# Kernel tuning notes

Hardware: AMD Instinct MI355X
Metric: run time of the kernel (lower is better)

## Reference

```python
import jax, jax.numpy as jnp
import numpy as np
import math

EMBED_DIM = 128
SCALE = math.sqrt(EMBED_DIM)


def setup_inputs() -> dict:
    key = jax.random.key(0)
    # x: [B, N, D, L] = [4, 16, 128, 2048]
    x = jax.random.normal(key, (4, 16, 128, 2048), dtype=jnp.float32)
    return {"x": x}


def reference(x):
    # x: [B, N, D, L] -> [B, N, L, D]
    xt = jnp.swapaxes(x, -1, -2)
    # scores: [B, N, L, L] = softmax(x x^T / sqrt(D))
    scores = jnp.einsum("bnld,bnmd->bnlm", xt, xt) / jnp.asarray(SCALE, xt.dtype)
    attn = jax.nn.softmax(scores, axis=-1)
    # weighted values then mean over query positions L -> [B, N, D]
    out = jnp.einsum("bnlm,bnmd->bnld", attn, xt).mean(axis=2)
    return out
```

## Files before the change

### kernel.cpp

```cpp
#include <hip/hip_runtime.h>
#include <hip/hip_fp16.h>

#define H_  64
#define D_  128
#define L_  2048
#define PRE 0.35709578f

typedef _Float16 half8 __attribute__((ext_vector_type(8)));
typedef float    f32x4 __attribute__((ext_vector_type(4)));

__device__ __forceinline__ float fast_exp2(float x) {
#if __has_builtin(__builtin_amdgcn_exp2f)
    return __builtin_amdgcn_exp2f(x);
#else
    return __builtin_exp2f(x);
#endif
}

__device__ __forceinline__ void gload16(const void* g, void* l) {
    __builtin_amdgcn_global_load_lds(
        (const __attribute__((address_space(1))) void*)g,
        (__attribute__((address_space(3))) void*)l,
        16, 0, 0);
}

__device__ __forceinline__ void stage32k(const char* __restrict__ src,
                                         char* __restrict__ dst,
                                         int wid, int lane) {
#pragma unroll
    for (int j = 0; j < 8; ++j) {
        const unsigned o   = (unsigned)(wid * 8 + j) * 1024u + (unsigned)lane * 16u;
        const unsigned row = o >> 8;
        const unsigned so  = (o & ~255u) | ((o & 255u) ^ ((row & 7u) << 4));
        gload16(src + so, dst + (size_t)(wid * 8 + j) * 1024u);
    }
}

__global__ __launch_bounds__(256) void k_transpose(const float* __restrict__ x,
                                                   __half* __restrict__ xt) {
    const int h  = blockIdx.x;
    const int lc = blockIdx.y;
    __shared__ float raw[128][65];
    const float* xh = x + (size_t)h * D_ * L_ + (size_t)lc * 64;
    const int t = threadIdx.x;
    const int r0 = t >> 4;
    const int c4 = (t & 15) << 2;
#pragma unroll
    for (int i = 0; i < 8; ++i) {
        const int d = i * 16 + r0;
        const float4 v = *(const float4*)(xh + (size_t)d * L_ + c4);
        raw[d][c4 + 0] = v.x; raw[d][c4 + 1] = v.y;
        raw[d][c4 + 2] = v.z; raw[d][c4 + 3] = v.w;
    }
    __syncthreads();
    const int lane = t & 63, w = t >> 6;
    __half2* xth = (__half2*)(xt + (size_t)h * L_ * D_ + (size_t)lc * 64 * D_);
#pragma unroll
    for (int i = 0; i < 16; ++i) {
        const int jl = w * 16 + i;
        const float a = raw[2 * lane][jl] * PRE;
        const float b = raw[2 * lane + 1][jl] * PRE;
        xth[(size_t)jl * 64 + lane] = __floats2half2_rn(a, b);
    }
}

template <int PASS>
__global__ __launch_bounds__(256, 2) void k_gemm(const __half* __restrict__ xt,
                                                 const float* __restrict__ ainv,
                                                 float* __restrict__ zw) {
    __shared__ char  smA[32768];
    __shared__ char  smB[32768];
    __shared__ float csum[2][128];
    __shared__ float zfin[2][128];

    const int bid = blockIdx.x;
    const int res = bid & 7;
    const int j   = bid >> 3;
    const int h   = ((j >> 3) << 3) | res;
    const int pid = j & 7;

    const int t    = threadIdx.x;
    const int lane = t & 63;
    const int wid  = t >> 6;
    const int wr   = wid >> 1, wc = wid & 1;
    const int lo   = lane & 15, hi = lane >> 4;
    const unsigned sx = (unsigned)((lane & 7) << 4);

    const char*  xh  = (const char*)(xt + (size_t)h * (L_ * D_));
    float*       zwh = zw + ((size_t)h * 17 << 11);
    const float* ah  = ainv + ((size_t)h << 11);

#pragma unroll 1
    for (int pp = 0; pp < 2; ++pp) {
        const int p   = pp ? (15 - pid) : pid;
        const int nst = 16 - p;

        stage32k(xh + (size_t)p * 32768, smA, wid, lane);

        float rs[4][4] = {};
        float ar[4][4];
        if (PASS == 2) {
#pragma unroll
            for (int fm = 0; fm < 4; ++fm)
#pragma unroll
                for (int r = 0; r < 4; ++r)
                    ar[fm][r] = ah[p * 128 + wr * 64 + fm * 16 + hi * 4 + r];
        }
        __syncthreads();

#pragma unroll 1
        for (int it = 0; it < nst; ++it) {
            const int ct = p + it;
            const char* tb;
            if (it == 0) {
                tb = smA;
            } else {
                stage32k(xh + (size_t)ct * 32768, smB, wid, lane);
                __syncthreads();
                tb = smB;
            }
            float acol[4];
            if (PASS == 2) {
#pragma unroll
                for (int fn = 0; fn < 4; ++fn)
                    acol[fn] = ah[ct * 128 + wc * 64 + fn * 16 + lo];
            }

            f32x4 acc[4][4] = {};
            __builtin_amdgcn_s_setprio(1);
#pragma unroll
            for (int s = 0; s < 4; ++s) {
                half8 a[4], b[4];
                const unsigned inr = ((unsigned)(s * 64 + hi * 16)) ^ sx;
#pragma unroll
                for (int f = 0; f < 4; ++f) {
                    a[f] = *(const half8*)(smA + (unsigned)(wr * 64 + f * 16 + lo) * 256 + inr);
                    b[f] = *(const half8*)(tb  + (unsigned)(wc * 64 + f * 16 + lo) * 256 + inr);
                }
#pragma unroll
                for (int fm = 0; fm < 4; ++fm)
#pragma unroll
                    for (int fn = 0; fn < 4; ++fn)
                        acc[fm][fn] = __builtin_amdgcn_mfma_f32_16x16x32_f16(
                            a[fm], b[fn], acc[fm][fn], 0, 0, 0);
            }
            __builtin_amdgcn_s_setprio(0);

            if (PASS == 1 && it == 0) {
#pragma unroll
                for (int fm = 0; fm < 4; ++fm)
#pragma unroll
                    for (int fn = 0; fn < 4; ++fn)
#pragma unroll
                        for (int r = 0; r < 4; ++r)
                            rs[fm][r] += fast_exp2(acc[fm][fn][r]);
            } else {
                float cs[4] = {0.f, 0.f, 0.f, 0.f};
#pragma unroll
                for (int fm = 0; fm < 4; ++fm)
#pragma unroll
                    for (int fn = 0; fn < 4; ++fn)
#pragma unroll
                        for (int r = 0; r < 4; ++r) {
                            const float e = fast_exp2(acc[fm][fn][r]);
                            if (PASS == 1) {
                                rs[fm][r] += e;
                                cs[fn]    += e;
                            } else {
                                cs[fn] += ar[fm][r] * e;
                                if (it > 0) rs[fm][r] += acol[fn] * e;
                            }
                        }
#pragma unroll
                for (int fn = 0; fn < 4; ++fn) {
                    cs[fn] += __shfl_xor(cs[fn], 16, 64);
                    cs[fn] += __shfl_xor(cs[fn], 32, 64);
                }
                if (lane < 16) {
#pragma unroll
                    for (int fn = 0; fn < 4; ++fn)
                        csum[wr][wc * 64 + fn * 16 + lane] = cs[fn];
                }
                __syncthreads();
                if (t < 128) {
                    const float s2 = csum[0][t] + csum[1][t];
                    const size_t o = ((size_t)ct << 7) + t;
                    if (PASS == 2 && it == 0) zwh[((size_t)16 << 11) + o] = s2;
                    else                      zwh[((size_t)p  << 11) + o] = s2;
                }
            }
        }

#pragma unroll
        for (int fm = 0; fm < 4; ++fm)
#pragma unroll
            for (int r = 0; r < 4; ++r) {
                float v = rs[fm][r];
                v += __shfl_xor(v, 1, 64);
                v += __shfl_xor(v, 2, 64);
                v += __shfl_xor(v, 4, 64);
                v += __shfl_xor(v, 8, 64);
                if (lo == 0) zfin[wc][wr * 64 + fm * 16 + hi * 4 + r] = v;
            }
        __syncthreads();
        if (t < 128)
            zwh[((size_t)15 << 11) + ((size_t)p << 7) + t] = zfin[0][t] + zfin[1][t];
        __syncthreads();
    }
}

__global__ __launch_bounds__(256) void k_reduceZ(const float* __restrict__ zp,
                                                 float* __restrict__ ainv) {
    const int i = blockIdx.x * 256 + threadIdx.x;
    const int h = i >> 11, l = i & 2047, q = l >> 7;
    float z = zp[(((size_t)h * 17 + 15) << 11) + l];
#pragma unroll
    for (int p = 0; p < 15; ++p)
        if (p < q) z += zp[(((size_t)h * 17 + p) << 11) + l];
    ainv[i] = 1.0f / z;
}

__global__ __launch_bounds__(256) void k_out(const float* __restrict__ x,
                                             const float* __restrict__ wp,
                                             float* __restrict__ out) {
    __shared__ float wl[L_];
    const int h = blockIdx.x >> 2, qb = blockIdx.x & 3;
    const int t = threadIdx.x, lane = t & 63, wid = t >> 6;
    for (int c = t; c < L_; c += 256) {
        const int q = c >> 7;
        float s = wp[(((size_t)h * 17 + 15) << 11) + c]
                + wp[(((size_t)h * 17 + 16) << 11) + c];
#pragma unroll
        for (int p = 0; p < 15; ++p)
            if (p < q) s += wp[(((size_t)h * 17 + p) << 11) + c];
        wl[c] = s;
    }
    __syncthreads();
#pragma unroll 1
    for (int it = 0; it < 8; ++it) {
        const int d = qb * 32 + wid * 8 + it;
        const float* xr = x + ((size_t)h * D_ + d) * L_;
        float s = 0.0f;
#pragma unroll
        for (int kk = 0; kk < 8; ++kk) {
            const int m = kk * 256 + lane * 4;
            const float4 xv = *(const float4*)(xr + m);
            const float4 wv = *(const float4*)(wl + m);
            s += xv.x * wv.x + xv.y * wv.y + xv.z * wv.z + xv.w * wv.w;
        }
#pragma unroll
        for (int dm = 1; dm < 64; dm <<= 1) s += __shfl_xor(s, dm, 64);
        if (lane == 0) out[(size_t)h * D_ + d] = s * (1.0f / (float)L_);
    }
}

extern "C" void kernel_launch(void* const* d_in, const int* in_sizes, int n_in,
                              void* d_out, int out_size, void* d_ws, size_t ws_size,
                              hipStream_t stream) {
    const float* x = (const float*)d_in[0];
    float* out = (float*)d_out;
    char* ws = (char*)d_ws;

    __half* xt  = (__half*)(ws);
    float* zwp  = (float*)(ws + 33554432);
    float* ainv = (float*)(ws + 33554432 + 8912896);

    k_transpose<<<dim3(H_, L_ / 64), 256, 0, stream>>>(x, xt);
    k_gemm<1><<<512, 256, 0, stream>>>(xt, ainv, zwp);
    k_reduceZ<<<(H_ * L_) / 256, 256, 0, stream>>>(zwp, ainv);
    k_gemm<2><<<512, 256, 0, stream>>>(xt, ainv, zwp);
    k_out<<<H_ * 4, 256, 0, stream>>>(x, zwp, out);
}
```

Baseline: 158.0 us.

## Double-buffer half-size column tiles with async prefetch and drop per-tile block sync

The GEMM kernel now streams column tiles as 16KB halves into a double buffer, prefetching the next half while computing the current one, with explicit vmcnt waits and raw barriers in place of __syncthreads. The per-tile column-sum reduction through shared memory and its block barrier are removed. Each warp-row now writes its partial sums directly to separate slots (33 slots instead of 17), and the reduce/output kernels sum the extra slots. PASS 2 also caches ainv in LDS, and exp2 switches to the generic builtin. In exchange, global workspace writes double and LDS use grows slightly, which may affect occupancy.

```diff
diff --git a/kernel.cpp b/kernel.cpp
--- a/kernel.cpp
+++ b/kernel.cpp
@@ -9,12 +9,13 @@
 typedef _Float16 half8 __attribute__((ext_vector_type(8)));
 typedef float    f32x4 __attribute__((ext_vector_type(4)));
 
-__device__ __forceinline__ float fast_exp2(float x) {
-#if __has_builtin(__builtin_amdgcn_exp2f)
-    return __builtin_amdgcn_exp2f(x);
-#else
-    return __builtin_exp2f(x);
-#endif
+#define SLOTS 33
+
+__device__ __forceinline__ float fast_exp2(float x) { return __builtin_exp2f(x); }
+
+template <int N>
+__device__ __forceinline__ void wait_vm() {
+    asm volatile("s_waitcnt vmcnt(%0)" :: "n"(N) : "memory");
 }
 
 __device__ __forceinline__ void gload16(const void* g, void* l) {
@@ -33,6 +34,18 @@
         const unsigned row = o >> 8;
         const unsigned so  = (o & ~255u) | ((o & 255u) ^ ((row & 7u) << 4));
         gload16(src + so, dst + (size_t)(wid * 8 + j) * 1024u);
+    }
+}
+
+__device__ __forceinline__ void stage16k(const char* __restrict__ src,
+                                         char* __restrict__ dst,
+                                         int wid, int lane) {
+#pragma unroll
+    for (int j = 0; j < 4; ++j) {
+        const unsigned o   = (unsigned)(wid * 4 + j) * 1024u + (unsigned)lane * 16u;
+        const unsigned row = o >> 8;
+        const unsigned so  = (o & ~255u) | ((o & 255u) ^ ((row & 7u) << 4));
+        gload16(src + so, dst + (size_t)(wid * 4 + j) * 1024u);
     }
 }
 
@@ -69,9 +82,9 @@
                                                  const float* __restrict__ ainv,
                                                  float* __restrict__ zw) {
     __shared__ char  smA[32768];
-    __shared__ char  smB[32768];
-    __shared__ float csum[2][128];
+    __shared__ char  smB[2][16384];
     __shared__ float zfin[2][128];
+    __shared__ float aS[2048];
 
     const int bid = blockIdx.x;
     const int res = bid & 7;
@@ -87,15 +100,24 @@
     const unsigned sx = (unsigned)((lane & 7) << 4);
 
     const char*  xh  = (const char*)(xt + (size_t)h * (L_ * D_));
-    float*       zwh = zw + ((size_t)h * 17 << 11);
+    float*       zwh = zw + (size_t)h * SLOTS * 2048;
     const float* ah  = ainv + ((size_t)h << 11);
+
+    if (PASS == 2) {
+        const float4* a4 = (const float4*)ah;
+        *(float4*)&aS[t * 8]     = a4[t * 2];
+        *(float4*)&aS[t * 8 + 4] = a4[t * 2 + 1];
+    }
 
 #pragma unroll 1
     for (int pp = 0; pp < 2; ++pp) {
         const int p   = pp ? (15 - pid) : pid;
         const int nst = 16 - p;
-
+        const int NS  = 2 * (nst - 1);
+
+        __syncthreads();
         stage32k(xh + (size_t)p * 32768, smA, wid, lane);
+        if (NS > 0) stage16k(xh + (size_t)(p + 1) * 32768, smB[0], wid, lane);
 
         float rs[4][4] = {};
         float ar[4][4];
@@ -104,62 +126,79 @@
             for (int fm = 0; fm < 4; ++fm)
 #pragma unroll
                 for (int r = 0; r < 4; ++r)
-                    ar[fm][r] = ah[p * 128 + wr * 64 + fm * 16 + hi * 4 + r];
+                    ar[fm][r] = aS[p * 128 + wr * 64 + fm * 16 + hi * 4 + r];
         }
-        __syncthreads();
+        if (NS == 0) {
+            wait_vm<0>();
+            __builtin_amdgcn_sched_barrier(0);
+            __builtin_amdgcn_s_barrier();
+            __builtin_amdgcn_sched_barrier(0);
+        }
 
 #pragma unroll 1
-        for (int it = 0; it < nst; ++it) {
-            const int ct = p + it;
-            const char* tb;
-            if (it == 0) {
-                tb = smA;
-            } else {
-                stage32k(xh + (size_t)ct * 32768, smB, wid, lane);
-                __syncthreads();
-                tb = smB;
-            }
-            float acol[4];
-            if (PASS == 2) {
-#pragma unroll
-                for (int fn = 0; fn < 4; ++fn)
-                    acol[fn] = ah[ct * 128 + wc * 64 + fn * 16 + lo];
-            }
-
-            f32x4 acc[4][4] = {};
+        for (int c = 0; c < 2 * nst; ++c) {
+            const bool isdiag = (c >= NS);
+            if (!isdiag) {
+                if (c + 1 < NS) {
+                    __builtin_amdgcn_s_barrier();
+                    __builtin_amdgcn_sched_barrier(0);
+                    stage16k(xh + (size_t)(p + 1) * 32768 + (size_t)(c + 1) * 16384,
+                             smB[(c + 1) & 1], wid, lane);
+                    wait_vm<4>();
+                } else {
+                    wait_vm<0>();
+                }
+                __builtin_amdgcn_sched_barrier(0);
+                __builtin_amdgcn_s_barrier();
+                __builtin_amdgcn_sched_barrier(0);
+            }
+
+            const char* tb = isdiag ? (smA + (size_t)(c - NS) * 16384)
+                                    : (const char*)smB[c & 1];
+            const int tc = isdiag ? p : (p + 1 + (c >> 1));
+            const int ch = isdiag ? (c - NS) : (c & 1);
+
+            float acol[2];
+            if (PASS == 2 && !isdiag) {
+                acol[0] = aS[tc * 128 + ch * 64 + wc * 32 + lo];
+                acol[1] = aS[tc * 128 + ch * 64 + wc * 32 + 16 + lo];
+            }
+
+            f32x4 acc[4][2] = {};
             __builtin_amdgcn_s_setprio(1);
 #pragma unroll
             for (int s = 0; s < 4; ++s) {
-                half8 a[4], b[4];
+                half8 a[4], b[2];
                 const unsigned inr = ((unsigned)(s * 64 + hi * 16)) ^ sx;
 #pragma unroll
-                for (int f = 0; f < 4; ++f) {
+                for (int f = 0; f < 4; ++f)
                     a[f] = *(const half8*)(smA + (unsigned)(wr * 64 + f * 16 + lo) * 256 + inr);
-                    b[f] = *(const half8*)(tb  + (unsigned)(wc * 64 + f * 16 + lo) * 256 + inr);
-                }
+#pragma unroll
+                for (int f = 0; f < 2; ++f)
+                    b[f] = *(const half8*)(tb + (unsigned)(wc * 32 + f * 16 + lo) * 256 + inr);
 #pragma unroll
                 for (int fm = 0; fm < 4; ++fm)
 #pragma unroll
-                    for (int fn = 0; fn < 4; ++fn)
+                    for (int fn = 0; fn < 2; ++fn)
                         acc[fm][fn] = __builtin_amdgcn_mfma_f32_16x16x32_f16(
                             a[fm], b[fn], acc[fm][fn], 0, 0, 0);
             }
             __builtin_amdgcn_s_setprio(0);
 
-            if (PASS == 1 && it == 0) {
+            if (PASS == 1 && isdiag) {
 #pragma unroll
                 for (int fm = 0; fm < 4; ++fm)
 #pragma unroll
-                    for (int fn = 0; fn < 4; ++fn)
+                    for (int fn = 0; fn < 2; ++fn)
 #pragma unroll
                         for (int r = 0; r < 4; ++r)
                             rs[fm][r] += fast_exp2(acc[fm][fn][r]);
             } else {
-                float cs[4] = {0.f, 0.f, 0.f, 0.f};
+                float cs[2] = {0.f, 0.f};
 #pragma unroll
                 for (int fm = 0; fm < 4; ++fm)
 #pragma unroll
-                    for (int fn = 0; fn < 4; ++fn)
+                    for (int fn = 0; fn < 2; ++fn)
 #pragma unroll
                         for (int r = 0; r < 4; ++r) {
                             const float e = fast_exp2(acc[fm][fn][r]);
@@ -168,25 +207,19 @@
                                 cs[fn]    += e;
                             } else {
                                 cs[fn] += ar[fm][r] * e;
-                                if (it > 0) rs[fm][r] += acol[fn] * e;
+                                if (!isdiag) rs[fm][r] += acol[fn] * e;
                             }
                         }
 #pragma unroll
-                for (int fn = 0; fn < 4; ++fn) {
+                for (int fn = 0; fn < 2; ++fn) {
                     cs[fn] += __shfl_xor(cs[fn], 16, 64);
                     cs[fn] += __shfl_xor(cs[fn], 32, 64);
                 }
-                if (lane < 16) {
-#pragma unroll
-                    for (int fn = 0; fn < 4; ++fn)
-                        csum[wr][wc * 64 + fn * 16 + lane] = cs[fn];
-                }
-                __syncthreads();
-                if (t < 128) {
-                    const float s2 = csum[0][t] + csum[1][t];
-                    const size_t o = ((size_t)ct << 7) + t;
-                    if (PASS == 2 && it == 0) zwh[((size_t)16 << 11) + o] = s2;
-                    else                      zwh[((size_t)p  << 11) + o] = s2;
+                if (hi == 0) {
+                    const int slot = isdiag ? (30 + wr) : (2 * p + wr);
+#pragma unroll
+                    for (int fn = 0; fn < 2; ++fn)
+                        zwh[((size_t)slot << 11) + tc * 128 + ch * 64 + wc * 32 + fn * 16 + lo] = cs[fn];
                 }
             }
         }
@@ -204,8 +237,7 @@
             }
         __syncthreads();
         if (t < 128)
-            zwh[((size_t)15 << 11) + ((size_t)p << 7) + t] = zfin[0][t] + zfin[1][t];
-        __syncthreads();
+            zwh[((size_t)32 << 11) + ((size_t)p << 7) + t] = zfin[0][t] + zfin[1][t];
     }
 }
 
@@ -213,10 +245,11 @@
                                                  float* __restrict__ ainv) {
     const int i = blockIdx.x * 256 + threadIdx.x;
     const int h = i >> 11, l = i & 2047, q = l >> 7;
-    float z = zp[(((size_t)h * 17 + 15) << 11) + l];
+    const float* zh = zp + (size_t)h * SLOTS * 2048;
+    float z = zh[((size_t)32 << 11) + l];
 #pragma unroll
     for (int p = 0; p < 15; ++p)
-        if (p < q) z += zp[(((size_t)h * 17 + p) << 11) + l];
+        if (p < q) z += zh[((size_t)(2 * p) << 11) + l] + zh[((size_t)(2 * p + 1) << 11) + l];
     ainv[i] = 1.0f / z;
 }
 
@@ -226,13 +259,15 @@
     __shared__ float wl[L_];
     const int h = blockIdx.x >> 2, qb = blockIdx.x & 3;
     const int t = threadIdx.x, lane = t & 63, wid = t >> 6;
+    const float* wh = wp + (size_t)h * SLOTS * 2048;
     for (int c = t; c < L_; c += 256) {
         const int q = c >> 7;
-        float s = wp[(((size_t)h * 17 + 15) << 11) + c]
-                + wp[(((size_t)h * 17 + 16) << 11) + c];
+        float s = wh[((size_t)32 << 11) + c]
+                + wh[((size_t)30 << 11) + c]
+                + wh[((size_t)31 << 11) + c];
 #pragma unroll
         for (int p = 0; p < 15; ++p)
-            if (p < q) s += wp[(((size_t)h * 17 + p) << 11) + c];
+            if (p < q) s += wh[((size_t)(2 * p) << 11) + c] + wh[((size_t)(2 * p + 1) << 11) + c];
         wl[c] = s;
     }
     __syncthreads();
@@ -263,7 +298,7 @@
 
     __half* xt  = (__half*)(ws);
     float* zwp  = (float*)(ws + 33554432);
-    float* ainv = (float*)(ws + 33554432 + 8912896);
+    float* ainv = (float*)(ws + 33554432 + 17301504);
 
     k_transpose<<<dim3(H_, L_ / 64), 256, 0, stream>>>(x, xt);
     k_gemm<1><<<512, 256, 0, stream>>>(xt, ainv, zwp);
```

Result: slower. 208.7 us (+32.1%).

## Double-buffer tile staging with 8-wave blocks and register-resident A fragments

Applied to the files above, without the earlier changes.

Reworks the GEMM kernel to 512-thread blocks in which each wave owns a 32-row slice of the query tile. The A fragments stay in registers for the whole pass, and the next key tile is prefetched into a second LDS buffer while the current one is computed. The column-sum writeback is deferred by one iteration through double-buffered csum, which removes one barrier per tile. The ainv vector is staged in LDS, and fast_exp2 switches to the generic exp2f builtin, which may add instructions. The added LDS footprint may limit occupancy, and the pass boundary drops a barrier that could race on csum.

```diff
diff --git a/kernel.cpp b/kernel.cpp
--- a/kernel.cpp
+++ b/kernel.cpp
@@ -5,17 +5,12 @@
 #define D_  128
 #define L_  2048
 #define PRE 0.35709578f
+#define SLOTS 17
 
 typedef _Float16 half8 __attribute__((ext_vector_type(8)));
 typedef float    f32x4 __attribute__((ext_vector_type(4)));
 
-__device__ __forceinline__ float fast_exp2(float x) {
-#if __has_builtin(__builtin_amdgcn_exp2f)
-    return __builtin_amdgcn_exp2f(x);
-#else
-    return __builtin_exp2f(x);
-#endif
-}
+__device__ __forceinline__ float fast_exp2(float x) { return __builtin_exp2f(x); }
 
 __device__ __forceinline__ void gload16(const void* g, void* l) {
     __builtin_amdgcn_global_load_lds(
@@ -24,15 +19,15 @@
         16, 0, 0);
 }
 
-__device__ __forceinline__ void stage32k(const char* __restrict__ src,
-                                         char* __restrict__ dst,
-                                         int wid, int lane) {
-#pragma unroll
-    for (int j = 0; j < 8; ++j) {
-        const unsigned o   = (unsigned)(wid * 8 + j) * 1024u + (unsigned)lane * 16u;
+__device__ __forceinline__ void stage32k8(const char* __restrict__ src,
+                                          char* __restrict__ dst,
+                                          int wid, int lane) {
+#pragma unroll
+    for (int jj = 0; jj < 4; ++jj) {
+        const unsigned o   = (unsigned)(wid * 4 + jj) * 1024u + (unsigned)lane * 16u;
         const unsigned row = o >> 8;
         const unsigned so  = (o & ~255u) | ((o & 255u) ^ ((row & 7u) << 4));
-        gload16(src + so, dst + (size_t)(wid * 8 + j) * 1024u);
+        gload16(src + so, dst + (size_t)(wid * 4 + jj) * 1024u);
     }
 }
 
@@ -65,12 +60,12 @@
 }
 
 template <int PASS>
-__global__ __launch_bounds__(256, 2) void k_gemm(const __half* __restrict__ xt,
+__global__ __launch_bounds__(512, 4) void k_gemm(const __half* __restrict__ xt,
                                                  const float* __restrict__ ainv,
                                                  float* __restrict__ zw) {
-    __shared__ char  smA[32768];
-    __shared__ char  smB[32768];
-    __shared__ float csum[2][128];
+    __shared__ char  sm[65536];
+    __shared__ float aS[2048];
+    __shared__ float csum[2][4][128];
     __shared__ float zfin[2][128];
 
     const int bid = blockIdx.x;
@@ -82,95 +77,99 @@
     const int t    = threadIdx.x;
     const int lane = t & 63;
     const int wid  = t >> 6;
-    const int wr   = wid >> 1, wc = wid & 1;
+    const int wr   = wid >> 1;
+    const int wc   = wid & 1;
     const int lo   = lane & 15, hi = lane >> 4;
-    const unsigned sx = (unsigned)((lane & 7) << 4);
-
-    const char*  xh  = (const char*)(xt + (size_t)h * (L_ * D_));
-    float*       zwh = zw + ((size_t)h * 17 << 11);
-    const float* ah  = ainv + ((size_t)h << 11);
+    const unsigned sx   = (unsigned)((lane & 7) << 4);
+    const unsigned rowA = (unsigned)(wr * 32 + lo);
+    const unsigned rowB = (unsigned)(wc * 64 + lo);
+
+    const char* xh  = (const char*)(xt + (size_t)h * (L_ * D_));
+    float*      zwh = zw + (size_t)h * SLOTS * 2048;
+
+    if (PASS == 2)
+        *(float4*)&aS[t * 4] = ((const float4*)(ainv + ((size_t)h << 11)))[t];
 
 #pragma unroll 1
     for (int pp = 0; pp < 2; ++pp) {
-        const int p   = pp ? (15 - pid) : pid;
-        const int nst = 16 - p;
-
-        stage32k(xh + (size_t)p * 32768, smA, wid, lane);
-
-        float rs[4][4] = {};
-        float ar[4][4];
+        const int p  = pp ? (15 - pid) : pid;
+        const int NS = 15 - p;
+
+        stage32k8(xh + (size_t)p * 32768, sm, wid, lane);
+        if (NS > 0) stage32k8(xh + (size_t)(p + 1) * 32768, sm + 32768, wid, lane);
+        __syncthreads();
+
+        half8 afr[2][4];
+#pragma unroll
+        for (int fm = 0; fm < 2; ++fm)
+#pragma unroll
+            for (int s = 0; s < 4; ++s)
+                afr[fm][s] = *(const half8*)(sm + (rowA + fm * 16) * 256
+                                                + (((unsigned)(s * 64 + hi * 16)) ^ sx));
+        float rs[2][4] = {};
+        float ar[2][4];
         if (PASS == 2) {
 #pragma unroll
-            for (int fm = 0; fm < 4; ++fm)
+            for (int fm = 0; fm < 2; ++fm)
 #pragma unroll
                 for (int r = 0; r < 4; ++r)
-                    ar[fm][r] = ah[p * 128 + wr * 64 + fm * 16 + hi * 4 + r];
-        }
-        __syncthreads();
+                    ar[fm][r] = aS[p * 128 + wr * 32 + fm * 16 + hi * 4 + r];
+        }
 
 #pragma unroll 1
-        for (int it = 0; it < nst; ++it) {
+        for (int it = 0; it <= NS; ++it) {
             const int ct = p + it;
-            const char* tb;
-            if (it == 0) {
-                tb = smA;
-            } else {
-                stage32k(xh + (size_t)ct * 32768, smB, wid, lane);
-                __syncthreads();
-                tb = smB;
-            }
+            if (it > 0) __syncthreads();
+            if (it < NS)
+                stage32k8(xh + (size_t)(ct + 1) * 32768,
+                          sm + (((it + 1) & 1) ? 32768 : 0), wid, lane);
+            if (it >= 1 && t < 128) {
+                const int pr = (it - 1) & 1;
+                const float v = csum[pr][0][t] + csum[pr][1][t]
+                              + csum[pr][2][t] + csum[pr][3][t];
+                if (it == 1) { if (PASS == 2) zwh[((size_t)16 << 11) + (size_t)p * 128 + t] = v; }
+                else         zwh[((size_t)p << 11) + (size_t)(ct - 1) * 128 + t] = v;
+            }
+
+            const char* bbuf = (it == 0) ? sm : (sm + ((it & 1) ? 32768 : 0));
             float acol[4];
             if (PASS == 2) {
 #pragma unroll
                 for (int fn = 0; fn < 4; ++fn)
-                    acol[fn] = ah[ct * 128 + wc * 64 + fn * 16 + lo];
-            }
-
-            f32x4 acc[4][4] = {};
+                    acol[fn] = aS[ct * 128 + wc * 64 + fn * 16 + lo];
+            }
+
+            f32x4 acc[2][4] = {};
             __builtin_amdgcn_s_setprio(1);
 #pragma unroll
             for (int s = 0; s < 4; ++s) {
-                half8 a[4], b[4];
                 const unsigned inr = ((unsigned)(s * 64 + hi * 16)) ^ sx;
-#pragma unroll
-                for (int f = 0; f < 4; ++f) {
-                    a[f] = *(const half8*)(smA + (unsigned)(wr * 64 + f * 16 + lo) * 256 + inr);
-                    b[f] = *(const half8*)(tb  + (unsigned)(wc * 64 + f * 16 + lo) * 256 + inr);
-                }
-#pragma unroll
-                for (int fm = 0; fm < 4; ++fm)
+                half8 b[4];
+#pragma unroll
+                for (int fn = 0; fn < 4; ++fn)
+                    b[fn] = *(const half8*)(bbuf + (rowB + fn * 16) * 256 + inr);
+#pragma unroll
+                for (int fm = 0; fm < 2; ++fm)
 #pragma unroll
                     for (int fn = 0; fn < 4; ++fn)
                         acc[fm][fn] = __builtin_amdgcn_mfma_f32_16x16x32_f16(
-                            a[fm], b[fn], acc[fm][fn], 0, 0, 0);
+                            afr[fm][s], b[fn], acc[fm][fn], 0, 0, 0);
             }
             __builtin_amdgcn_s_setprio(0);
 
-            if (PASS == 1 && it == 0) {
-#pragma unroll
-                for (int fm = 0; fm < 4; ++fm)
-#pragma unroll
-                    for (int fn = 0; fn < 4; ++fn)
-#pragma unroll
-                        for (int r = 0; r < 4; ++r)
-                            rs[fm][r] += fast_exp2(acc[fm][fn][r]);
-            } else {
-                float cs[4] = {0.f, 0.f, 0.f, 0.f};
-#pragma unroll
-                for (int fm = 0; fm < 4; ++fm)
-#pragma unroll
-                    for (int fn = 0; fn < 4; ++fn)
-#pragma unroll
-                        for (int r = 0; r < 4; ++r) {
-                            const float e = fast_exp2(acc[fm][fn][r]);
-                            if (PASS == 1) {
-                                rs[fm][r] += e;
-                                cs[fn]    += e;
-                            } else {
-                                cs[fn] += ar[fm][r] * e;
-                                if (it > 0) rs[fm][r] += acol[fn] * e;
-                            }
-                        }
+            float cs[4] = {0.f, 0.f, 0.f, 0.f};
+#pragma unroll
+            for (int fm = 0; fm < 2; ++fm)
+#pragma unroll
+                for (int fn = 0; fn < 4; ++fn)
+#pragma unroll
+                    for (int r = 0; r < 4; ++r) {
+                        const float e = fast_exp2(acc[fm][fn][r]);
+                        if (PASS == 1) { rs[fm][r] += e; cs[fn] += e; }
+                        else           { cs[fn] += ar[fm][r] * e;
+                                         if (it > 0) rs[fm][r] += acol[fn] * e; }
+                    }
+            if (!(PASS == 1 && it == 0)) {
 #pragma unroll
                 for (int fn = 0; fn < 4; ++fn) {
                     cs[fn] += __shfl_xor(cs[fn], 16, 64);
@@ -179,20 +178,13 @@
                 if (lane < 16) {
 #pragma unroll
                     for (int fn = 0; fn < 4; ++fn)
-                        csum[wr][wc * 64 + fn * 16 + lane] = cs[fn];
+                        csum[it & 1][wr][wc * 64 + fn * 16 + lane] = cs[fn];
                 }
-                __syncthreads();
-                if (t < 128) {
-                    const float s2 = csum[0][t] + csum[1][t];
-                    const size_t o = ((size_t)ct << 7) + t;
-                    if (PASS == 2 && it == 0) zwh[((size_t)16 << 11) + o] = s2;
-                    else                      zwh[((size_t)p  << 11) + o] = s2;
-                }
-            }
-        }
-
-#pragma unroll
-        for (int fm = 0; fm < 4; ++fm)
+            }
+        }
+
+#pragma unroll
+        for (int fm = 0; fm < 2; ++fm)
 #pragma unroll
             for (int r = 0; r < 4; ++r) {
                 float v = rs[fm][r];
@@ -200,12 +192,17 @@
                 v += __shfl_xor(v, 2, 64);
                 v += __shfl_xor(v, 4, 64);
                 v += __shfl_xor(v, 8, 64);
-                if (lo == 0) zfin[wc][wr * 64 + fm * 16 + hi * 4 + r] = v;
+                if (lo == 0) zfin[wc][wr * 32 + fm * 16 + hi * 4 + r] = v;
             }
         __syncthreads();
-        if (t < 128)
+        if (t < 128) {
             zwh[((size_t)15 << 11) + ((size_t)p << 7) + t] = zfin[0][t] + zfin[1][t];
-        __syncthreads();
+            const int pr = NS & 1;
+            const float v = csum[pr][0][t] + csum[pr][1][t]
+                          + csum[pr][2][t] + csum[pr][3][t];
+            if (NS == 0) { if (PASS == 2) zwh[((size_t)16 << 11) + (size_t)p * 128 + t] = v; }
+            else         zwh[((size_t)p << 11) + (size_t)(p + NS) * 128 + t] = v;
+        }
     }
 }
 
@@ -213,10 +210,11 @@
                                                  float* __restrict__ ainv) {
     const int i = blockIdx.x * 256 + threadIdx.x;
     const int h = i >> 11, l = i & 2047, q = l >> 7;
-    float z = zp[(((size_t)h * 17 + 15) << 11) + l];
+    const float* zh = zp + (size_t)h * SLOTS * 2048;
+    float z = zh[((size_t)15 << 11) + l];
 #pragma unroll
     for (int p = 0; p < 15; ++p)
-        if (p < q) z += zp[(((size_t)h * 17 + p) << 11) + l];
+        if (p < q) z += zh[((size_t)p << 11) + l];
     ainv[i] = 1.0f / z;
 }
 
@@ -226,13 +224,13 @@
     __shared__ float wl[L_];
     const int h = blockIdx.x >> 2, qb = blockIdx.x & 3;
     const int t = threadIdx.x, lane = t & 63, wid = t >> 6;
+    const float* wh = wp + (size_t)h * SLOTS * 2048;
     for (int c = t; c < L_; c += 256) {
         const int q = c >> 7;
-        float s = wp[(((size_t)h * 17 + 15) << 11) + c]
-                + wp[(((size_t)h * 17 + 16) << 11) + c];
+        float s = wh[((size_t)15 << 11) + c] + wh[((size_t)16 << 11) + c];
 #pragma unroll
         for (int p = 0; p < 15; ++p)
-            if (p < q) s += wp[(((size_t)h * 17 + p) << 11) + c];
+            if (p < q) s += wh[((size_t)p << 11) + c];
         wl[c] = s;
     }
     __syncthreads();
@@ -266,8 +264,8 @@
     float* ainv = (float*)(ws + 33554432 + 8912896);
 
     k_transpose<<<dim3(H_, L_ / 64), 256, 0, stream>>>(x, xt);
-    k_gemm<1><<<512, 256, 0, stream>>>(xt, ainv, zwp);
+    k_gemm<1><<<512, 512, 0, stream>>>(xt, ainv, zwp);
     k_reduceZ<<<(H_ * L_) / 256, 256, 0, stream>>>(zwp, ainv);
-    k_gemm<2><<<512, 256, 0, stream>>>(xt, ainv, zwp);
+    k_gemm<2><<<512, 512, 0, stream>>>(xt, ainv, zwp);
     k_out<<<H_ * 4, 256, 0, stream>>>(x, zwp, out);
 }
```

Result: slower. 231.8 us (+46.7%).
